# Kernel tuning notes

Hardware: AMD Instinct MI355X
Metric: run time of the kernel (lower is better)

The kernel has to match this reference:

```python
import jax, jax.numpy as jnp
import numpy as np

D_MODEL = 2048
N_HEADS = 16
D_HEAD = D_MODEL // N_HEADS  # 128
WINDOW = 512
SCALE = D_HEAD ** -0.5


def setup_inputs() -> dict:
    key = jax.random.key(0)
    ks = jax.random.split(key, 5)
    B, S = 2, 4096
    x = jax.random.normal(ks[0], (B, S, D_MODEL), dtype=jnp.float32)
    W_qkv = jax.random.normal(ks[1], (D_MODEL, 3 * D_MODEL), dtype=jnp.float32) * (D_MODEL ** -0.5)
    b_qkv = jax.random.normal(ks[2], (3 * D_MODEL,), dtype=jnp.float32) * 0.02
    W_out = jax.random.normal(ks[3], (D_MODEL, D_MODEL), dtype=jnp.float32) * (D_MODEL ** -0.5)
    b_out = jax.random.normal(ks[4], (D_MODEL,), dtype=jnp.float32) * 0.02
    return {"x": x, "W_qkv": W_qkv, "b_qkv": b_qkv, "W_out": W_out, "b_out": b_out}


def reference(x, W_qkv, b_qkv, W_out, b_out):
    B, S, D = x.shape
    nb = S // WINDOW  # number of independent causal windows (block-diagonal attention)
    qkv = x @ W_qkv + b_qkv  # (B,S,3D)
    q, k, v = jnp.split(qkv, 3, axis=-1)

    def to_blocks(t):
        # (B,S,D) -> (B,H,nb,W,dh)
        return t.reshape(B, nb, WINDOW, N_HEADS, D_HEAD).transpose(0, 3, 1, 2, 4)

    q, k, v = to_blocks(q), to_blocks(k), to_blocks(v)
    # per-window attention scores: (B,H,nb,W,W)
    scores = jnp.einsum('bhnqd,bhnkd->bhnqk', q, k) * SCALE
    causal = jnp.tril(jnp.ones((WINDOW, WINDOW), dtype=bool))
    scores = jnp.where(causal, scores, -jnp.inf)
    attn = jax.nn.softmax(scores, axis=-1)
    out = jnp.einsum('bhnqk,bhnkd->bhnqd', attn, v)  # (B,H,nb,W,dh)
    out = out.transpose(0, 2, 3, 1, 4).reshape(B, S, D)
    return out @ W_out + b_out
```

## Files before the change

### kernel.cpp

```cpp
#include <hip/hip_runtime.h>
#include <stdint.h>


typedef unsigned short u16;
typedef unsigned int u32;
typedef __attribute__((ext_vector_type(8))) short bf16x8;
typedef __attribute__((ext_vector_type(4))) float f32x4;

#define QKVN 6144
#define DM 2048

__device__ __forceinline__ u16 f2b(float f) {
  u32 u = __builtin_bit_cast(u32, f);
  u32 r = (u + 0x7fffu + ((u >> 16) & 1u)) >> 16;
  return (u16)r;
}

__device__ __forceinline__ u32 pack_hi16(float hi, float lo) {
  return __builtin_amdgcn_perm(__builtin_bit_cast(u32, hi),
                               __builtin_bit_cast(u32, lo), 0x07060302u);
}

__device__ __forceinline__ float fexp2(float x) { return __builtin_amdgcn_exp2f(x); }

__device__ __forceinline__ void gload_lds16(const void* g, void* l) {
  __builtin_amdgcn_global_load_lds((const __attribute__((address_space(1))) void*)g,
                                   (__attribute__((address_space(3))) void*)l,
                                   16, 0, 0);
}


__global__ void cast_f32_bf16(const float4* __restrict__ x, uint4* __restrict__ o) {
  int idx = blockIdx.x * 256 + threadIdx.x;
  float4 a = x[2 * idx];
  float4 b = x[2 * idx + 1];
  uint4 r;
  r.x = (u32)f2b(a.x) | ((u32)f2b(a.y) << 16);
  r.y = (u32)f2b(a.z) | ((u32)f2b(a.w) << 16);
  r.z = (u32)f2b(b.x) | ((u32)f2b(b.y) << 16);
  r.w = (u32)f2b(b.z) | ((u32)f2b(b.w) << 16);
  o[idx] = r;
}

__global__ void transpose_cast(const float* __restrict__ W, u16* __restrict__ Wt,
                               int K, int N) {
  __shared__ u16 tile[64][65];
  int tx = threadIdx.x & 63;
  int ty = threadIdx.x >> 6;
  int n0 = blockIdx.x * 64;
  int k0 = blockIdx.y * 64;
#pragma unroll
  for (int r = 0; r < 64; r += 4)
    tile[r + ty][tx] = f2b(W[(size_t)(k0 + r + ty) * N + n0 + tx]);
  __syncthreads();
#pragma unroll
  for (int r = 0; r < 64; r += 4)
    Wt[(size_t)(n0 + r + ty) * K + k0 + tx] = tile[tx][r + ty];
}


template <typename TO>
__global__ __launch_bounds__(256, 2) void gemm_bt(const u16* __restrict__ A,
                                                  const u16* __restrict__ Bt,
                                                  const float* __restrict__ bias,
                                                  TO* __restrict__ C,
                                                  int M, int N, int K) {
  __shared__ u16 As[128 * 64];
  __shared__ u16 Bs[256 * 64];
  const int tid = threadIdx.x;
  const int lane = tid & 63;
  const int wave = tid >> 6;
  const int quad = lane >> 4;
  const int l15 = lane & 15;
  const int m0 = blockIdx.y * 128;
  const int n0 = blockIdx.x * 256;
  const int wm = (wave & 1) * 64;
  const int wn = (wave >> 1) * 128;

  f32x4 acc[4][8] = {};

  for (int k0 = 0; k0 < K; k0 += 64) {
#pragma unroll
    for (int i = 0; i < 4; ++i) {
      int sb = wave * 256 + i * 64;
      int s = sb + lane;
      int m = s >> 3;
      int c = (s & 7) ^ (m & 7);
      gload_lds16(A + (size_t)(m0 + m) * K + (k0 + c * 8), As + sb * 8);
    }
#pragma unroll
    for (int i = 0; i < 8; ++i) {
      int sb = wave * 512 + i * 64;
      int s = sb + lane;
      int n = s >> 3;
      int c = (s & 7) ^ (n & 7);
      gload_lds16(Bt + (size_t)(n0 + n) * K + (k0 + c * 8), Bs + sb * 8);
    }
    __syncthreads();
#pragma unroll
    for (int ks = 0; ks < 2; ++ks) {
      bf16x8 af[4], bf[8];
#pragma unroll
      for (int i = 0; i < 4; ++i) {
        int m = wm + i * 16 + l15;
        af[i] = *(const bf16x8*)(As + m * 64 + (((ks * 4 + quad) ^ (m & 7)) << 3));
      }
#pragma unroll
      for (int j = 0; j < 8; ++j) {
        int n = wn + j * 16 + l15;
        bf[j] = *(const bf16x8*)(Bs + n * 64 + (((ks * 4 + quad) ^ (n & 7)) << 3));
      }
#pragma unroll
      for (int i = 0; i < 4; ++i)
#pragma unroll
        for (int j = 0; j < 8; ++j)
          acc[i][j] = __builtin_amdgcn_mfma_f32_16x16x32_bf16(af[i], bf[j], acc[i][j], 0, 0, 0);
    }
    __syncthreads();
  }

#pragma unroll
  for (int j = 0; j < 8; ++j) {
    int col = n0 + wn + j * 16 + l15;
    float bv = bias[col];
#pragma unroll
    for (int i = 0; i < 4; ++i) {
      int row = m0 + wm + i * 16 + quad * 4;
#pragma unroll
      for (int t = 0; t < 4; ++t) {
        float v = acc[i][j][t] + bv;
        if constexpr (sizeof(TO) == 2)
          C[(size_t)(row + t) * N + col] = (TO)f2b(v);
        else
          C[(size_t)(row + t) * N + col] = (TO)v;
      }
    }
  }
}


template <bool MASK>
__device__ __forceinline__ void attn_step(
    int jt, int tid, int wave, int quad, int l15, int qt, int tokw, int h,
    const u16* __restrict__ qkv, u16* Vt, u16* Ps,
    const bf16x8 (&qf)[2][4], f32x4 (&acc_o)[8][2], float (&mrun)[2],
    float (&lrun)[2]) {
  const float SL2E = 0.12751745f;
  u16* VtB = Vt + (jt & 1) * (128 * 64);
  u16* PsB = Ps + (jt & 1) * (128 * 64);

  const u16* Vb = qkv + (size_t)(tokw + jt * 64) * QKVN + 4096 + h * 128;
  const int p = tid & 31;
  const int dc0 = tid >> 5;
  const int kk0 = p * 2;
  const u16* g0 = Vb + (size_t)kk0 * QKVN + dc0 * 8;
  uint4 vr0 = *(const uint4*)g0;
  uint4 vr1 = *(const uint4*)(g0 + QKVN);
  uint4 vr2 = *(const uint4*)(g0 + 64);
  uint4 vr3 = *(const uint4*)(g0 + QKVN + 64);

  f32x4 acc_s[4][2] = {};
  {
    const u16* Kb = qkv + (size_t)(tokw + jt * 64) * QKVN + 2048 + h * 128;
    bf16x8 kf[4][4];
#pragma unroll
    for (int i = 0; i < 4; ++i) {
      const u16* Kr = Kb + (size_t)(i * 16 + l15) * QKVN + quad * 8;
#pragma unroll
      for (int ks = 0; ks < 4; ++ks)
        kf[i][ks] = *(const bf16x8*)(Kr + ks * 32);
    }
#pragma unroll
    for (int ks = 0; ks < 4; ++ks)
#pragma unroll
      for (int i = 0; i < 4; ++i)
#pragma unroll
        for (int j = 0; j < 2; ++j)
          acc_s[i][j] = __builtin_amdgcn_mfma_f32_16x16x32_bf16(kf[i][ks], qf[j][ks],
                                                                acc_s[i][j], 0, 0, 0);
  }

  {
    const u16* a0 = (const u16*)&vr0;
    const u16* a1 = (const u16*)&vr1;
    const u16* a2 = (const u16*)&vr2;
    const u16* a3 = (const u16*)&vr3;
    int c = kk0 >> 3;
    int boff = (kk0 & 7) << 1;
#pragma unroll
    for (int j = 0; j < 8; ++j) {
      int d = dc0 * 8 + j;
      *(u32*)((char*)VtB + d * 128 + ((c ^ (d & 7)) << 4) + boff) =
          (u32)a0[j] | ((u32)a1[j] << 16);
      int d2 = d + 64;
      *(u32*)((char*)VtB + d2 * 128 + ((c ^ (d2 & 7)) << 4) + boff) =
          (u32)a2[j] | ((u32)a3[j] << 16);
    }
  }

#pragma unroll
  for (int j = 0; j < 2; ++j) {
    int ql = wave * 32 + j * 16 + l15;
    float vmax = -1e30f;
#pragma unroll
    for (int i = 0; i < 4; ++i)
#pragma unroll
      for (int t = 0; t < 4; ++t) {
        float s = acc_s[i][j][t];
        if (MASK) {
          int kg = jt * 64 + i * 16 + quad * 4 + t;
          if (kg > qt * 128 + ql) s = -1e30f;
          acc_s[i][j][t] = s;
        }
        vmax = fmaxf(vmax, s);
      }
    vmax = fmaxf(vmax, __shfl_xor(vmax, 16));
    vmax = fmaxf(vmax, __shfl_xor(vmax, 32));
    float mnew = fmaxf(mrun[j], vmax * SL2E);
    float alpha = fexp2(mrun[j] - mnew);
    mrun[j] = mnew;
    float vsum = 0.f;
#pragma unroll
    for (int i = 0; i < 4; ++i) {
      float p0 = fexp2(__builtin_fmaf(acc_s[i][j][0], SL2E, -mnew));
      float p1 = fexp2(__builtin_fmaf(acc_s[i][j][1], SL2E, -mnew));
      float p2 = fexp2(__builtin_fmaf(acc_s[i][j][2], SL2E, -mnew));
      float p3 = fexp2(__builtin_fmaf(acc_s[i][j][3], SL2E, -mnew));
      vsum += (p0 + p1) + (p2 + p3);
      uint2 pk;
      pk.x = pack_hi16(p1, p0);
      pk.y = pack_hi16(p3, p2);
      int kk = i * 16 + quad * 4;
      *(uint2*)((char*)PsB + ql * 128 + (((kk >> 3) ^ (ql & 7)) << 4) + ((kk & 7) << 1)) = pk;
    }
    vsum += __shfl_xor(vsum, 16);
    vsum += __shfl_xor(vsum, 32);
    lrun[j] = lrun[j] * alpha + vsum;
    if (__ballot(alpha < 0.99995f)) {
#pragma unroll
      for (int i2 = 0; i2 < 8; ++i2)
#pragma unroll
        for (int t = 0; t < 4; ++t)
          acc_o[i2][j][t] *= alpha;
    }
  }
  __syncthreads();

#pragma unroll
  for (int ks = 0; ks < 2; ++ks) {
    int kc = ks * 4 + quad;
    bf16x8 pf[2];
#pragma unroll
    for (int j = 0; j < 2; ++j) {
      int ql = wave * 32 + j * 16 + l15;
      pf[j] = *(const bf16x8*)((char*)PsB + ql * 128 + ((kc ^ (ql & 7)) << 4));
    }
#pragma unroll
    for (int i2 = 0; i2 < 8; ++i2) {
      int d = i2 * 16 + l15;
      bf16x8 vf = *(const bf16x8*)((char*)VtB + d * 128 + ((kc ^ (d & 7)) << 4));
#pragma unroll
      for (int j = 0; j < 2; ++j)
        acc_o[i2][j] = __builtin_amdgcn_mfma_f32_16x16x32_bf16(vf, pf[j], acc_o[i2][j], 0, 0, 0);
    }
  }
}

__global__ __launch_bounds__(256, 2) void attn_win(const u16* __restrict__ qkv,
                                                   u16* __restrict__ attn_out) {
  __shared__ u16 Vt[2 * 128 * 64];
  __shared__ u16 Ps[2 * 128 * 64];
  const int tid = threadIdx.x;
  const int lane = tid & 63;
  const int wave = tid >> 6;
  const int quad = lane >> 4;
  const int l15 = lane & 15;
  const int qt = blockIdx.x;
  const int win = blockIdx.y;
  const int b = blockIdx.z >> 4;
  const int h = blockIdx.z & 15;
  const int tokw = b * 4096 + win * 512;
  const int tokq = tokw + qt * 128;

  bf16x8 qf[2][4];
  {
    const u16* Qb = qkv + (size_t)tokq * QKVN + h * 128;
#pragma unroll
    for (int j = 0; j < 2; ++j) {
      const u16* Qr = Qb + (size_t)(wave * 32 + j * 16 + l15) * QKVN + quad * 8;
#pragma unroll
      for (int ks = 0; ks < 4; ++ks)
        qf[j][ks] = *(const bf16x8*)(Qr + ks * 32);
    }
  }

  f32x4 acc_o[8][2] = {};
  float mrun[2] = {-1e30f, -1e30f};
  float lrun[2] = {0.f, 0.f};

  int jt = 0;
  const int diag = 2 * qt;
  for (; jt < diag; ++jt)
    attn_step<false>(jt, tid, wave, quad, l15, qt, tokw, h, qkv, Vt, Ps, qf, acc_o, mrun, lrun);
  for (; jt <= diag + 1; ++jt)
    attn_step<true>(jt, tid, wave, quad, l15, qt, tokw, h, qkv, Vt, Ps, qf, acc_o, mrun, lrun);

#pragma unroll
  for (int j = 0; j < 2; ++j) {
    float inv = 1.0f / lrun[j];
    int ql = wave * 32 + j * 16 + l15;
    u16* orow = attn_out + (size_t)(tokq + ql) * DM + h * 128;
#pragma unroll
    for (int i2 = 0; i2 < 8; ++i2) {
      int d = i2 * 16 + quad * 4;
      uint2 pk;
      pk.x = (u32)f2b(acc_o[i2][j][0] * inv) | ((u32)f2b(acc_o[i2][j][1] * inv) << 16);
      pk.y = (u32)f2b(acc_o[i2][j][2] * inv) | ((u32)f2b(acc_o[i2][j][3] * inv) << 16);
      *(uint2*)(orow + d) = pk;
    }
  }
}


extern "C" void kernel_launch(void* const* d_in, const int* in_sizes, int n_in,
                              void* d_out, int out_size, void* d_ws, size_t ws_size,
                              hipStream_t stream) {
  const float* x = (const float*)d_in[0];
  const float* W_qkv = (const float*)d_in[1];
  const float* b_qkv = (const float*)d_in[2];
  const float* W_out = (const float*)d_in[3];
  const float* b_out = (const float*)d_in[4];
  float* out = (float*)d_out;

  char* w = (char*)d_ws;
  u16* xb = (u16*)w;
  u16* wqkvT = (u16*)(w + 33554432);
  u16* woutT = (u16*)(w + 33554432 + 25165824);
  u16* qkv = (u16*)(w + 67108864);

  cast_f32_bf16<<<8192, 256, 0, stream>>>((const float4*)x, (uint4*)xb);
  transpose_cast<<<dim3(96, 32), 256, 0, stream>>>(W_qkv, wqkvT, 2048, 6144);
  transpose_cast<<<dim3(32, 32), 256, 0, stream>>>(W_out, woutT, 2048, 2048);
  gemm_bt<u16><<<dim3(24, 64), 256, 0, stream>>>(xb, wqkvT, b_qkv, qkv, 8192, 6144, 2048);
  attn_win<<<dim3(4, 8, 32), 256, 0, stream>>>(qkv, xb);
  gemm_bt<float><<<dim3(8, 64), 256, 0, stream>>>(xb, woutT, b_out, out, 8192, 2048, 2048);
}
```

Baseline: 532.9 us.

## Restructure GEMMs: register double-buffered B tile, direct global A loads, smaller tiles

The GEMM kernel now uses 128x128 tiles instead of 128x256. B is staged through a double-buffered LDS tile that is prefetched into registers one k-step ahead, and A fragments are read straight from global memory instead of through LDS. The async global_load_lds path and one barrier per k-step are gone, and occupancy rises to three blocks per CU. The risk is that uncoalesced direct global A loads, plus less reuse from the smaller tiles, raise memory traffic and latency.

```diff
diff --git a/kernel.cpp b/kernel.cpp
--- a/kernel.cpp
+++ b/kernel.cpp
@@ -22,12 +22,6 @@
 }
 
 __device__ __forceinline__ float fexp2(float x) { return __builtin_amdgcn_exp2f(x); }
-
-__device__ __forceinline__ void gload_lds16(const void* g, void* l) {
-  __builtin_amdgcn_global_load_lds((const __attribute__((address_space(1))) void*)g,
-                                   (__attribute__((address_space(3))) void*)l,
-                                   16, 0, 0);
-}
 
 
 __global__ void cast_f32_bf16(const float4* __restrict__ x, uint4* __restrict__ o) {
@@ -60,67 +54,91 @@
 
 
 template <typename TO>
-__global__ __launch_bounds__(256, 2) void gemm_bt(const u16* __restrict__ A,
-                                                  const u16* __restrict__ Bt,
-                                                  const float* __restrict__ bias,
-                                                  TO* __restrict__ C,
-                                                  int M, int N, int K) {
-  __shared__ u16 As[128 * 64];
-  __shared__ u16 Bs[256 * 64];
+__device__ __forceinline__ void gemm_body(u16* __restrict__ Bs,
+                                          const u16* __restrict__ A,
+                                          const u16* __restrict__ Bt,
+                                          const float* __restrict__ bias,
+                                          TO* __restrict__ C,
+                                          int M, int N, int K) {
   const int tid = threadIdx.x;
   const int lane = tid & 63;
   const int wave = tid >> 6;
   const int quad = lane >> 4;
   const int l15 = lane & 15;
   const int m0 = blockIdx.y * 128;
-  const int n0 = blockIdx.x * 256;
+  const int n0 = blockIdx.x * 128;
   const int wm = (wave & 1) * 64;
-  const int wn = (wave >> 1) * 128;
-
-  f32x4 acc[4][8] = {};
-
-  for (int k0 = 0; k0 < K; k0 += 64) {
-#pragma unroll
-    for (int i = 0; i < 4; ++i) {
-      int sb = wave * 256 + i * 64;
-      int s = sb + lane;
-      int m = s >> 3;
-      int c = (s & 7) ^ (m & 7);
-      gload_lds16(A + (size_t)(m0 + m) * K + (k0 + c * 8), As + sb * 8);
-    }
-#pragma unroll
-    for (int i = 0; i < 8; ++i) {
-      int sb = wave * 512 + i * 64;
-      int s = sb + lane;
-      int n = s >> 3;
-      int c = (s & 7) ^ (n & 7);
-      gload_lds16(Bt + (size_t)(n0 + n) * K + (k0 + c * 8), Bs + sb * 8);
+  const int wn = (wave >> 1) * 64;
+  const int NK = K >> 6;
+
+  int srow[4], scc[4];
+#pragma unroll
+  for (int i = 0; i < 4; ++i) {
+    int c = i * 256 + tid;
+    srow[i] = c >> 3;
+    scc[i] = c & 7;
+  }
+
+  f32x4 acc[4][4] = {};
+
+  {
+    uint4 bs[4];
+#pragma unroll
+    for (int i = 0; i < 4; ++i)
+      bs[i] = *(const uint4*)(Bt + (size_t)(n0 + srow[i]) * K + scc[i] * 8);
+#pragma unroll
+    for (int i = 0; i < 4; ++i)
+      *(uint4*)(Bs + srow[i] * 64 + ((scc[i] ^ (srow[i] & 7)) << 3)) = bs[i];
+  }
+  __syncthreads();
+
+  for (int k = 0; k < NK; ++k) {
+    u16* cur = Bs + (k & 1) * (128 * 64);
+    u16* nxt = Bs + ((k + 1) & 1) * (128 * 64);
+    const bool more = (k + 1 < NK);
+    const int k1 = (k + 1) << 6;
+
+    uint4 bsn[4];
+    if (more) {
+#pragma unroll
+      for (int i = 0; i < 4; ++i)
+        bsn[i] = *(const uint4*)(Bt + (size_t)(n0 + srow[i]) * K + k1 + scc[i] * 8);
+    }
+
+    const int kk = k << 6;
+    bf16x8 af[4][2];
+#pragma unroll
+    for (int ks = 0; ks < 2; ++ks)
+#pragma unroll
+      for (int i = 0; i < 4; ++i)
+        af[i][ks] = *(const bf16x8*)(A + (size_t)(m0 + wm + i * 16 + l15) * K + kk +
+                                     ks * 32 + quad * 8);
+
+#pragma unroll
+    for (int ks = 0; ks < 2; ++ks) {
+      bf16x8 bf[4];
+#pragma unroll
+      for (int j = 0; j < 4; ++j) {
+        int n = wn + j * 16 + l15;
+        bf[j] = *(const bf16x8*)(cur + n * 64 + (((ks * 4 + quad) ^ (n & 7)) << 3));
+      }
+#pragma unroll
+      for (int i = 0; i < 4; ++i)
+#pragma unroll
+        for (int j = 0; j < 4; ++j)
+          acc[i][j] = __builtin_amdgcn_mfma_f32_16x16x32_bf16(af[i][ks], bf[j], acc[i][j], 0, 0, 0);
+    }
+
+    if (more) {
+#pragma unroll
+      for (int i = 0; i < 4; ++i)
+        *(uint4*)(nxt + srow[i] * 64 + ((scc[i] ^ (srow[i] & 7)) << 3)) = bsn[i];
     }
     __syncthreads();
-#pragma unroll
-    for (int ks = 0; ks < 2; ++ks) {
-      bf16x8 af[4], bf[8];
-#pragma unroll
-      for (int i = 0; i < 4; ++i) {
-        int m = wm + i * 16 + l15;
-        af[i] = *(const bf16x8*)(As + m * 64 + (((ks * 4 + quad) ^ (m & 7)) << 3));
-      }
-#pragma unroll
-      for (int j = 0; j < 8; ++j) {
-        int n = wn + j * 16 + l15;
-        bf[j] = *(const bf16x8*)(Bs + n * 64 + (((ks * 4 + quad) ^ (n & 7)) << 3));
-      }
-#pragma unroll
-      for (int i = 0; i < 4; ++i)
-#pragma unroll
-        for (int j = 0; j < 8; ++j)
-          acc[i][j] = __builtin_amdgcn_mfma_f32_16x16x32_bf16(af[i], bf[j], acc[i][j], 0, 0, 0);
-    }
-    __syncthreads();
-  }
-
-#pragma unroll
-  for (int j = 0; j < 8; ++j) {
+  }
+
+#pragma unroll
+  for (int j = 0; j < 4; ++j) {
     int col = n0 + wn + j * 16 + l15;
     float bv = bias[col];
 #pragma unroll
@@ -136,6 +154,24 @@
       }
     }
   }
+}
+
+__global__ __launch_bounds__(256, 3) void gemm_qkv(const u16* __restrict__ A,
+                                                   const u16* __restrict__ Bt,
+                                                   const float* __restrict__ bias,
+                                                   u16* __restrict__ C,
+                                                   int M, int N, int K) {
+  __shared__ u16 Bs[2 * 128 * 64];
+  gemm_body<u16>(Bs, A, Bt, bias, C, M, N, K);
+}
+
+__global__ __launch_bounds__(256, 3) void gemm_out(const u16* __restrict__ A,
+                                                   const u16* __restrict__ Bt,
+                                                   const float* __restrict__ bias,
+                                                   float* __restrict__ C,
+                                                   int M, int N, int K) {
+  __shared__ u16 Bs[2 * 128 * 64];
+  gemm_body<float>(Bs, A, Bt, bias, C, M, N, K);
 }
 
 
@@ -341,7 +377,7 @@
   cast_f32_bf16<<<8192, 256, 0, stream>>>((const float4*)x, (uint4*)xb);
   transpose_cast<<<dim3(96, 32), 256, 0, stream>>>(W_qkv, wqkvT, 2048, 6144);
   transpose_cast<<<dim3(32, 32), 256, 0, stream>>>(W_out, woutT, 2048, 2048);
-  gemm_bt<u16><<<dim3(24, 64), 256, 0, stream>>>(xb, wqkvT, b_qkv, qkv, 8192, 6144, 2048);
+  gemm_qkv<<<dim3(48, 64), 256, 0, stream>>>(xb, wqkvT, b_qkv, qkv, 8192, 6144, 2048);
   attn_win<<<dim3(4, 8, 32), 256, 0, stream>>>(qkv, xb);
-  gemm_bt<float><<<dim3(8, 64), 256, 0, stream>>>(xb, woutT, b_out, out, 8192, 2048, 2048);
-}
+  gemm_out<<<dim3(16, 64), 256, 0, stream>>>(xb, woutT, b_out, out, 8192, 2048, 2048);
+}
```

Measured after the change: 1.196 ms. +124.4%, slower.
